# Performance work log

Hardware: AMD Instinct MI355X
Metric: run time of the kernel (lower is better)

The kernel has to match this reference:

```python
import jax, jax.numpy as jnp
import numpy as np

EMBED = 1024
HEAD = 64
SEQ = 2048
BATCH = 8


def setup_inputs() -> dict:
    key = jax.random.key(0)
    kx, kq, kk, kv = jax.random.split(key, 4)
    x = jax.random.normal(kx, (BATCH, SEQ, EMBED), dtype=jnp.float32)
    # torch nn.Linear weight is [out,in]; we store [in,out] so y = x @ W
    Wq = jax.random.normal(kq, (EMBED, HEAD), dtype=jnp.float32) * (EMBED ** -0.5)
    Wk = jax.random.normal(kk, (EMBED, HEAD), dtype=jnp.float32) * (EMBED ** -0.5)
    Wv = jax.random.normal(kv, (EMBED, HEAD), dtype=jnp.float32) * (EMBED ** -0.5)
    return {"x": x, "Wq": Wq, "Wk": Wk, "Wv": Wv}


def reference(x, Wq, Wk, Wv):
    # x: [B,T,C]; single-head causal attention. Scale uses C (embedding dim),
    # matching the original module's C ** (-0.5). Dropout in eval mode (identity).
    B, T, C = x.shape
    q = x @ Wq  # [B,T,H]
    k = x @ Wk  # [B,T,H]
    v = x @ Wv  # [B,T,H]
    scores = jnp.einsum('bqh,bkh->bqk', q, k) * (C ** -0.5)  # [B,T,T]
    causal = jnp.tril(jnp.ones((T, T), dtype=bool))
    scores = jnp.where(causal, scores, -jnp.inf)
    weights = jax.nn.softmax(scores, axis=-1)
    return jnp.einsum('bqk,bkh->bqh', weights, v)  # [B,T,H]
```

## Files before the change

### kernel.cpp

```cpp
#include <hip/hip_runtime.h>
#include <hip/hip_bf16.h>
#include <math.h>

#define BATCH 8
#define SEQ 2048
#define EMBED 1024
#define HEAD 64
#define NROWS (BATCH*SEQ)

typedef short bf16x8 __attribute__((ext_vector_type(8)));
typedef short bf16x4 __attribute__((ext_vector_type(4)));
typedef float f32x4  __attribute__((ext_vector_type(4)));

__device__ inline short f2bf(float f) {
    __hip_bfloat16 h = __float2bfloat16(f);
    return *(short*)&h;
}
__device__ inline float bf2f(short s) {
    __hip_bfloat16 h = *(__hip_bfloat16*)&s;
    return __bfloat162float(h);
}

#define NSLOT 144
__device__ __host__ inline int triOff(int qt) {
    int g = qt >> 2;
    return 2 * g * (g + 1) + (qt & 3) * (g + 1);
}

__global__ __launch_bounds__(256) void prep_w(
    const float* __restrict__ Wq, const float* __restrict__ Wk,
    const float* __restrict__ Wv, short* __restrict__ wt)
{
    int g    = blockIdx.x * 256 + threadIdx.x;
    int lane = g & 63;
    int frag = g >> 6;
    int k32  = frag & 31;
    int ct   = frag >> 5;
    int col  = ct * 16 + (lane & 15);
    int mm   = col >> 6, cc = col & 63;
    const float* W = (mm == 0) ? Wq : ((mm == 1) ? Wk : Wv);
    int kb = k32 * 32 + (lane >> 4) * 8;
    bf16x8 o;
#pragma unroll
    for (int j = 0; j < 8; j++)
        o[j] = f2bf(W[(size_t)(kb + j) * HEAD + cc]);
    *(bf16x8*)&wt[(size_t)g * 8] = o;
}

__global__ __launch_bounds__(512, 4) void proj_kernel(
    const float* __restrict__ x, const short* __restrict__ wt,
    short* __restrict__ q, short* __restrict__ k, short* __restrict__ v)
{
    __shared__ short xs[32][1024];
    float* psum = (float*)&xs[0][0];

    const int tid  = threadIdx.x;
    const int wave = tid >> 6, lane = tid & 63;
    const int m16  = lane & 15, quad = lane >> 4;
    const int cg   = wave & 3;
    const int kh   = wave >> 2;
    const int r0   = blockIdx.x * 32;

    {
        const int row  = tid >> 4;
        const int col4 = tid & 15;
        const float* xr = x + (size_t)(r0 + row) * EMBED;
#pragma unroll
        for (int h = 0; h < 2; h++) {
            float4 f[8];
#pragma unroll
            for (int i = 0; i < 8; i++)
                f[i] = *(const float4*)&xr[(h * 8 + i) * 64 + col4 * 4];
#pragma unroll
            for (int i = 0; i < 8; i++) {
                int c  = (h * 8 + i) * 64 + col4 * 4;
                int k8 = c >> 3, rem = c & 7;
                int cs = ((k8 ^ (row & 7)) << 3) + rem;
                bf16x4 bv;
                bv[0] = f2bf(f[i].x); bv[1] = f2bf(f[i].y);
                bv[2] = f2bf(f[i].z); bv[3] = f2bf(f[i].w);
                *(bf16x4*)&xs[row][cs] = bv;
            }
        }
    }
    __syncthreads();

    f32x4 acc[2][3];
#pragma unroll
    for (int mt = 0; mt < 2; mt++)
#pragma unroll
        for (int j = 0; j < 3; j++) acc[mt][j] = (f32x4){0.f, 0.f, 0.f, 0.f};

#pragma unroll 4
    for (int s = 0; s < 16; s++) {
        int k32  = kh * 16 + s;
        int ksw  = ((k32 * 4 + quad) ^ (m16 & 7)) << 3;
        bf16x8 a0 = *(const bf16x8*)&xs[m16][ksw];
        bf16x8 a1 = *(const bf16x8*)&xs[16 + m16][ksw];
#pragma unroll
        for (int j = 0; j < 3; j++) {
            int ct = cg * 3 + j;
            bf16x8 bb = *(const bf16x8*)&wt[(size_t)((ct * 32 + k32) * 64 + lane) * 8];
            acc[0][j] = __builtin_amdgcn_mfma_f32_16x16x32_bf16(a0, bb, acc[0][j], 0, 0, 0);
            acc[1][j] = __builtin_amdgcn_mfma_f32_16x16x32_bf16(a1, bb, acc[1][j], 0, 0, 0);
        }
    }

    __syncthreads();
    if (kh == 1) {
        float* p = psum + ((size_t)(cg * 64 + lane) * 24);
#pragma unroll
        for (int mt = 0; mt < 2; mt++)
#pragma unroll
            for (int j = 0; j < 3; j++)
                *(f32x4*)&p[(mt * 3 + j) * 4] = acc[mt][j];
    }
    __syncthreads();
    if (kh == 0) {
        const float* p = psum + ((size_t)(cg * 64 + lane) * 24);
#pragma unroll
        for (int mt = 0; mt < 2; mt++)
#pragma unroll
            for (int j = 0; j < 3; j++) {
                f32x4 o = acc[mt][j] + *(const f32x4*)&p[(mt * 3 + j) * 4];
                int gcol = (cg * 3 + j) * 16 + m16;
                int mm = gcol >> 6, cc = gcol & 63;
                short* op = (mm == 0) ? q : ((mm == 1) ? k : v);
#pragma unroll
                for (int reg = 0; reg < 4; reg++) {
                    int row = r0 + mt * 16 + quad * 4 + reg;
                    op[(size_t)row * HEAD + cc] = f2bf(o[reg]);
                }
            }
    }
}

__global__ __launch_bounds__(256) void attn_kernel(
    const short* __restrict__ qg, const short* __restrict__ kg,
    const short* __restrict__ vg,
    short* __restrict__ pO, float* __restrict__ pl)
{
    __shared__ short ksh[64][88];
    __shared__ short vsh[64][88];
    __shared__ short psh[4][16][88];

    const int qt  = blockIdx.x;
    const int seg = blockIdx.y;
    const int b   = blockIdx.z;
    const int c0  = seg * 4;
    const int c1  = min(seg * 4 + 4, qt + 1);
    if (c0 >= c1) return;

    const int tid  = threadIdx.x;
    const int wave = tid >> 6, lane = tid & 63;
    const int m16  = lane & 15, quad = lane >> 4;
    const float scale = 0.03125f;

    const short* qb = qg + (size_t)b * SEQ * HEAD;
    const short* kb = kg + (size_t)b * SEQ * HEAD;
    const short* vb = vg + (size_t)b * SEQ * HEAD;

    bf16x8 a_q[2];
    {
        const int qrow = qt * 64 + wave * 16 + m16;
        a_q[0] = *(const bf16x8*)&qb[(size_t)qrow * HEAD + quad * 8];
        a_q[1] = *(const bf16x8*)&qb[(size_t)qrow * HEAD + 32 + quad * 8];
    }

    f32x4 o_acc[4];
#pragma unroll
    for (int i = 0; i < 4; i++) o_acc[i] = (f32x4){0.f, 0.f, 0.f, 0.f};
    float lsum[4] = {0.f, 0.f, 0.f, 0.f};

    const int krow = tid >> 3;
    const int ks8  = tid & 7;
    const int vp0  = tid >> 3;
    const int vh0  = (tid & 7) * 8;
    const int vpp  = vp0 ^ ((tid & 7) << 2);

    bf16x8 kr0 = *(const bf16x8*)&kb[(size_t)(c0 * 64 + krow) * HEAD + ks8 * 8];
    bf16x8 kr1 = *(const bf16x8*)&kb[(size_t)(c0 * 64 + 32 + krow) * HEAD + ks8 * 8];
    bf16x8 vr0 = *(const bf16x8*)&vb[(size_t)(c0 * 64 + 2 * vp0) * HEAD + vh0];
    bf16x8 vr1 = *(const bf16x8*)&vb[(size_t)(c0 * 64 + 2 * vp0 + 1) * HEAD + vh0];

    for (int c = c0; c < c1; c++) {
        const int t0 = c * 64;
        __syncthreads();
        {
            *(bf16x8*)&ksh[krow][ks8 * 8]      = kr0;
            *(bf16x8*)&ksh[32 + krow][ks8 * 8] = kr1;
#pragma unroll
            for (int j = 0; j < 8; j++) {
                int hh = vh0 + j;
                int val = (vr0[j] & 0xffff) | (((int)vr1[j]) << 16);
                *(int*)&vsh[hh][vpp * 2] = val;
            }
        }
        __syncthreads();
        if (c + 1 < c1) {
            const int tn = (c + 1) * 64;
            kr0 = *(const bf16x8*)&kb[(size_t)(tn + krow) * HEAD + ks8 * 8];
            kr1 = *(const bf16x8*)&kb[(size_t)(tn + 32 + krow) * HEAD + ks8 * 8];
            vr0 = *(const bf16x8*)&vb[(size_t)(tn + 2 * vp0) * HEAD + vh0];
            vr1 = *(const bf16x8*)&vb[(size_t)(tn + 2 * vp0 + 1) * HEAD + vh0];
        }

        f32x4 s_t[4];
#pragma unroll
        for (int nt = 0; nt < 4; nt++) {
            bf16x8 bk0 = *(const bf16x8*)&ksh[nt * 16 + m16][quad * 8];
            bf16x8 bk1 = *(const bf16x8*)&ksh[nt * 16 + m16][32 + quad * 8];
            f32x4 acc = (f32x4){0.f, 0.f, 0.f, 0.f};
            acc = __builtin_amdgcn_mfma_f32_16x16x32_bf16(a_q[0], bk0, acc, 0, 0, 0);
            acc = __builtin_amdgcn_mfma_f32_16x16x32_bf16(a_q[1], bk1, acc, 0, 0, 0);
            s_t[nt] = acc;
        }

        if (c == qt) {
#pragma unroll
            for (int r = 0; r < 4; r++) {
                const int row = qt * 64 + wave * 16 + quad * 4 + r;
#pragma unroll
                for (int nt = 0; nt < 4; nt++) {
                    int t = t0 + nt * 16 + m16;
                    float p = (t <= row) ? __expf(s_t[nt][r] * scale) : 0.f;
                    lsum[r] += p;
                    psh[wave][quad * 4 + r][nt * 16 + m16] = f2bf(p);
                }
            }
        } else {
#pragma unroll
            for (int r = 0; r < 4; r++) {
#pragma unroll
                for (int nt = 0; nt < 4; nt++) {
                    float p = __expf(s_t[nt][r] * scale);
                    lsum[r] += p;
                    psh[wave][quad * 4 + r][nt * 16 + m16] = f2bf(p);
                }
            }
        }

#pragma unroll
        for (int s = 0; s < 2; s++) {
            bf16x8 a_p = *(const bf16x8*)&psh[wave][m16][s * 32 + quad * 8];
#pragma unroll
            for (int ht = 0; ht < 4; ht++) {
                int hh = ht * 16 + m16;
                int pb = (s * 16 + quad * 4) ^ (((hh >> 3) & 7) << 2);
                bf16x8 b_v = *(const bf16x8*)&vsh[hh][pb * 2];
                o_acc[ht] = __builtin_amdgcn_mfma_f32_16x16x32_bf16(a_p, b_v, o_acc[ht], 0, 0, 0);
            }
        }
    }

#pragma unroll
    for (int r = 0; r < 4; r++) {
#pragma unroll
        for (int off = 8; off >= 1; off >>= 1)
            lsum[r] += __shfl_xor(lsum[r], off, 64);
    }
    const size_t slot  = (size_t)b * NSLOT + triOff(qt) + seg;
    const size_t pbase = slot * 64;
#pragma unroll
    for (int ht = 0; ht < 4; ht++) {
#pragma unroll
        for (int r = 0; r < 4; r++) {
            int rowt = wave * 16 + quad * 4 + r;
            pO[(pbase + rowt) * 64 + ht * 16 + m16] = f2bf(o_acc[ht][r]);
        }
    }
    if (m16 == 0) {
#pragma unroll
        for (int r = 0; r < 4; r++) {
            int rowt = wave * 16 + quad * 4 + r;
            pl[pbase + rowt] = lsum[r];
        }
    }
}

__global__ __launch_bounds__(256) void combine_kernel(
    const short* __restrict__ pO, const float* __restrict__ pl,
    float* __restrict__ out)
{
    int g   = blockIdx.x * 256 + threadIdx.x;
    int h4  = (g & 15) * 4;
    int row = (g >> 4) & 2047;
    int b   = g >> 15;
    int qt  = row >> 6, lr = row & 63;
    int ns  = (qt >> 2) + 1;
    size_t base = (size_t)b * NSLOT + triOff(qt);
    float4 O = {0.f, 0.f, 0.f, 0.f};
    float  L = 0.f;
    for (int s = 0; s < ns; s++) {
        bf16x4 ov = *(const bf16x4*)&pO[((base + s) * 64 + lr) * 64 + h4];
        O.x += bf2f(ov[0]); O.y += bf2f(ov[1]);
        O.z += bf2f(ov[2]); O.w += bf2f(ov[3]);
        L += pl[(base + s) * 64 + lr];
    }
    float inv = 1.f / L;
    O.x *= inv; O.y *= inv; O.z *= inv; O.w *= inv;
    *(float4*)&out[(size_t)g * 4] = O;
}

extern "C" void kernel_launch(void* const* d_in, const int* in_sizes, int n_in,
                              void* d_out, int out_size, void* d_ws, size_t ws_size,
                              hipStream_t stream) {
    const float* x  = (const float*)d_in[0];
    const float* Wq = (const float*)d_in[1];
    const float* Wk = (const float*)d_in[2];
    const float* Wv = (const float*)d_in[3];
    float* out = (float*)d_out;

    short* q  = (short*)d_ws;
    short* k  = q + (size_t)NROWS * HEAD;
    short* v  = k + (size_t)NROWS * HEAD;
    short* wt = v + (size_t)NROWS * HEAD;
    short* pO = wt + 196608;
    float* pl = (float*)(pO + (size_t)BATCH * NSLOT * 64 * 64);

    prep_w<<<96, 256, 0, stream>>>(Wq, Wk, Wv, wt);
    proj_kernel<<<512, 512, 0, stream>>>(x, wt, q, k, v);
    attn_kernel<<<dim3(32, 8, 8), 256, 0, stream>>>(q, k, v, pO, pl);
    combine_kernel<<<1024, 256, 0, stream>>>(pO, pl, out);
}
```

Baseline: 128.9 us.

## Store V transposed and read K/V directly from global, dropping LDS staging

The projection kernel now writes V in a transposed [B,H,T] layout, so the attention kernel can load V fragments for the PV MFMA directly from global memory with contiguous vector loads. The LDS staging of K and V, along with the per-tile __syncthreads barriers, is removed and each wave reads K/V itself through the cache. Partial outputs are re-indexed per 16-row wave tile. This removes block barriers and LDS traffic, but every wave in a block now fetches the same K/V tiles redundantly from L1/L2, and the transposed V store in proj is a 4-element strided write.

```diff
diff --git a/kernel.cpp b/kernel.cpp
--- a/kernel.cpp
+++ b/kernel.cpp
@@ -21,10 +21,10 @@
     return __bfloat162float(h);
 }
 
-#define NSLOT 144
-__device__ __host__ inline int triOff(int qt) {
-    int g = qt >> 2;
-    return 2 * g * (g + 1) + (qt & 3) * (g + 1);
+#define NSLOT16 576
+__device__ inline int triOff16(int qtile) {
+    int g = qtile >> 4;
+    return qtile + 8 * g * (g - 1) + (qtile & 15) * g;
 }
 
 __global__ __launch_bounds__(256) void prep_w(
@@ -49,7 +49,7 @@
 
 __global__ __launch_bounds__(512, 4) void proj_kernel(
     const float* __restrict__ x, const short* __restrict__ wt,
-    short* __restrict__ q, short* __restrict__ k, short* __restrict__ v)
+    short* __restrict__ q, short* __restrict__ k, short* __restrict__ vt)
 {
     __shared__ short xs[32][1024];
     float* psum = (float*)&xs[0][0];
@@ -118,6 +118,8 @@
     __syncthreads();
     if (kh == 0) {
         const float* p = psum + ((size_t)(cg * 64 + lane) * 24);
+        const int bb = r0 >> 11;
+        const int tb = r0 & 2047;
 #pragma unroll
         for (int mt = 0; mt < 2; mt++)
 #pragma unroll
@@ -125,11 +127,19 @@
                 f32x4 o = acc[mt][j] + *(const f32x4*)&p[(mt * 3 + j) * 4];
                 int gcol = (cg * 3 + j) * 16 + m16;
                 int mm = gcol >> 6, cc = gcol & 63;
-                short* op = (mm == 0) ? q : ((mm == 1) ? k : v);
-#pragma unroll
-                for (int reg = 0; reg < 4; reg++) {
-                    int row = r0 + mt * 16 + quad * 4 + reg;
-                    op[(size_t)row * HEAD + cc] = f2bf(o[reg]);
+                if (mm < 2) {
+                    short* op = (mm == 0) ? q : k;
+#pragma unroll
+                    for (int reg = 0; reg < 4; reg++) {
+                        int row = r0 + mt * 16 + quad * 4 + reg;
+                        op[(size_t)row * HEAD + cc] = f2bf(o[reg]);
+                    }
+                } else {
+                    bf16x4 pk;
+                    pk[0] = f2bf(o[0]); pk[1] = f2bf(o[1]);
+                    pk[2] = f2bf(o[2]); pk[3] = f2bf(o[3]);
+                    int t = tb + mt * 16 + quad * 4;
+                    *(bf16x4*)&vt[(((size_t)bb * 64 + cc) << 11) + t] = pk;
                 }
             }
     }
@@ -137,34 +147,32 @@
 
 __global__ __launch_bounds__(256) void attn_kernel(
     const short* __restrict__ qg, const short* __restrict__ kg,
-    const short* __restrict__ vg,
+    const short* __restrict__ vtg,
     short* __restrict__ pO, float* __restrict__ pl)
 {
-    __shared__ short ksh[64][88];
-    __shared__ short vsh[64][88];
-    __shared__ short psh[4][16][88];
-
-    const int qt  = blockIdx.x;
-    const int seg = blockIdx.y;
-    const int b   = blockIdx.z;
-    const int c0  = seg * 4;
-    const int c1  = min(seg * 4 + 4, qt + 1);
+    __shared__ short psh[4][16][72];
+
+    const int qt64 = blockIdx.x;
+    const int seg  = blockIdx.y;
+    const int b    = blockIdx.z;
+    const int c0 = seg * 4;
+    const int c1 = min(seg * 4 + 4, qt64 + 1);
     if (c0 >= c1) return;
 
-    const int tid  = threadIdx.x;
-    const int wave = tid >> 6, lane = tid & 63;
+    const int wave = threadIdx.x >> 6, lane = threadIdx.x & 63;
     const int m16  = lane & 15, quad = lane >> 4;
+    const int qtile = qt64 * 4 + wave;
     const float scale = 0.03125f;
 
-    const short* qb = qg + (size_t)b * SEQ * HEAD;
-    const short* kb = kg + (size_t)b * SEQ * HEAD;
-    const short* vb = vg + (size_t)b * SEQ * HEAD;
-
-    bf16x8 a_q[2];
+    const short* qb  = qg  + (size_t)b * SEQ * HEAD;
+    const short* kb  = kg  + (size_t)b * SEQ * HEAD;
+    const short* vtb = vtg + (size_t)b * HEAD * SEQ;
+
+    bf16x8 a_q0, a_q1;
     {
-        const int qrow = qt * 64 + wave * 16 + m16;
-        a_q[0] = *(const bf16x8*)&qb[(size_t)qrow * HEAD + quad * 8];
-        a_q[1] = *(const bf16x8*)&qb[(size_t)qrow * HEAD + 32 + quad * 8];
+        const int qrow = qtile * 16 + m16;
+        a_q0 = *(const bf16x8*)&qb[(size_t)qrow * HEAD + quad * 8];
+        a_q1 = *(const bf16x8*)&qb[(size_t)qrow * HEAD + 32 + quad * 8];
     }
 
     f32x4 o_acc[4];
@@ -172,54 +180,25 @@
     for (int i = 0; i < 4; i++) o_acc[i] = (f32x4){0.f, 0.f, 0.f, 0.f};
     float lsum[4] = {0.f, 0.f, 0.f, 0.f};
 
-    const int krow = tid >> 3;
-    const int ks8  = tid & 7;
-    const int vp0  = tid >> 3;
-    const int vh0  = (tid & 7) * 8;
-    const int vpp  = vp0 ^ ((tid & 7) << 2);
-
-    bf16x8 kr0 = *(const bf16x8*)&kb[(size_t)(c0 * 64 + krow) * HEAD + ks8 * 8];
-    bf16x8 kr1 = *(const bf16x8*)&kb[(size_t)(c0 * 64 + 32 + krow) * HEAD + ks8 * 8];
-    bf16x8 vr0 = *(const bf16x8*)&vb[(size_t)(c0 * 64 + 2 * vp0) * HEAD + vh0];
-    bf16x8 vr1 = *(const bf16x8*)&vb[(size_t)(c0 * 64 + 2 * vp0 + 1) * HEAD + vh0];
-
     for (int c = c0; c < c1; c++) {
         const int t0 = c * 64;
-        __syncthreads();
-        {
-            *(bf16x8*)&ksh[krow][ks8 * 8]      = kr0;
-            *(bf16x8*)&ksh[32 + krow][ks8 * 8] = kr1;
-#pragma unroll
-            for (int j = 0; j < 8; j++) {
-                int hh = vh0 + j;
-                int val = (vr0[j] & 0xffff) | (((int)vr1[j]) << 16);
-                *(int*)&vsh[hh][vpp * 2] = val;
-            }
-        }
-        __syncthreads();
-        if (c + 1 < c1) {
-            const int tn = (c + 1) * 64;
-            kr0 = *(const bf16x8*)&kb[(size_t)(tn + krow) * HEAD + ks8 * 8];
-            kr1 = *(const bf16x8*)&kb[(size_t)(tn + 32 + krow) * HEAD + ks8 * 8];
-            vr0 = *(const bf16x8*)&vb[(size_t)(tn + 2 * vp0) * HEAD + vh0];
-            vr1 = *(const bf16x8*)&vb[(size_t)(tn + 2 * vp0 + 1) * HEAD + vh0];
-        }
 
         f32x4 s_t[4];
 #pragma unroll
         for (int nt = 0; nt < 4; nt++) {
-            bf16x8 bk0 = *(const bf16x8*)&ksh[nt * 16 + m16][quad * 8];
-            bf16x8 bk1 = *(const bf16x8*)&ksh[nt * 16 + m16][32 + quad * 8];
+            const short* kr = &kb[(size_t)(t0 + nt * 16 + m16) * HEAD + quad * 8];
+            bf16x8 bk0 = *(const bf16x8*)kr;
+            bf16x8 bk1 = *(const bf16x8*)(kr + 32);
             f32x4 acc = (f32x4){0.f, 0.f, 0.f, 0.f};
-            acc = __builtin_amdgcn_mfma_f32_16x16x32_bf16(a_q[0], bk0, acc, 0, 0, 0);
-            acc = __builtin_amdgcn_mfma_f32_16x16x32_bf16(a_q[1], bk1, acc, 0, 0, 0);
+            acc = __builtin_amdgcn_mfma_f32_16x16x32_bf16(a_q0, bk0, acc, 0, 0, 0);
+            acc = __builtin_amdgcn_mfma_f32_16x16x32_bf16(a_q1, bk1, acc, 0, 0, 0);
             s_t[nt] = acc;
         }
 
-        if (c == qt) {
+        if (c == qt64) {
 #pragma unroll
             for (int r = 0; r < 4; r++) {
-                const int row = qt * 64 + wave * 16 + quad * 4 + r;
+                const int row = qtile * 16 + quad * 4 + r;
 #pragma unroll
                 for (int nt = 0; nt < 4; nt++) {
                     int t = t0 + nt * 16 + m16;
@@ -246,8 +225,7 @@
 #pragma unroll
             for (int ht = 0; ht < 4; ht++) {
                 int hh = ht * 16 + m16;
-                int pb = (s * 16 + quad * 4) ^ (((hh >> 3) & 7) << 2);
-                bf16x8 b_v = *(const bf16x8*)&vsh[hh][pb * 2];
+                bf16x8 b_v = *(const bf16x8*)&vtb[((size_t)hh << 11) + t0 + s * 32 + quad * 8];
                 o_acc[ht] = __builtin_amdgcn_mfma_f32_16x16x32_bf16(a_p, b_v, o_acc[ht], 0, 0, 0);
             }
         }
@@ -259,20 +237,20 @@
         for (int off = 8; off >= 1; off >>= 1)
             lsum[r] += __shfl_xor(lsum[r], off, 64);
     }
-    const size_t slot  = (size_t)b * NSLOT + triOff(qt) + seg;
-    const size_t pbase = slot * 64;
+    const size_t slot = (size_t)b * NSLOT16 + triOff16(qtile) + (seg - 0);
+    const size_t pbase = slot * 16;
 #pragma unroll
     for (int ht = 0; ht < 4; ht++) {
 #pragma unroll
         for (int r = 0; r < 4; r++) {
-            int rowt = wave * 16 + quad * 4 + r;
+            int rowt = quad * 4 + r;
             pO[(pbase + rowt) * 64 + ht * 16 + m16] = f2bf(o_acc[ht][r]);
         }
     }
     if (m16 == 0) {
 #pragma unroll
         for (int r = 0; r < 4; r++) {
-            int rowt = wave * 16 + quad * 4 + r;
+            int rowt = quad * 4 + r;
             pl[pbase + rowt] = lsum[r];
         }
     }
@@ -282,20 +260,20 @@
     const short* __restrict__ pO, const float* __restrict__ pl,
     float* __restrict__ out)
 {
-    int g   = blockIdx.x * 256 + threadIdx.x;
-    int h4  = (g & 15) * 4;
-    int row = (g >> 4) & 2047;
-    int b   = g >> 15;
-    int qt  = row >> 6, lr = row & 63;
-    int ns  = (qt >> 2) + 1;
-    size_t base = (size_t)b * NSLOT + triOff(qt);
+    int g    = blockIdx.x * 256 + threadIdx.x;
+    int h4   = (g & 15) * 4;
+    int row  = (g >> 4) & 2047;
+    int b    = g >> 15;
+    int qtile = row >> 4, rowt = row & 15;
+    int ns   = (qtile >> 4) + 1;
+    size_t base = (size_t)b * NSLOT16 + triOff16(qtile);
     float4 O = {0.f, 0.f, 0.f, 0.f};
     float  L = 0.f;
     for (int s = 0; s < ns; s++) {
-        bf16x4 ov = *(const bf16x4*)&pO[((base + s) * 64 + lr) * 64 + h4];
+        bf16x4 ov = *(const bf16x4*)&pO[((base + s) * 16 + rowt) * 64 + h4];
         O.x += bf2f(ov[0]); O.y += bf2f(ov[1]);
         O.z += bf2f(ov[2]); O.w += bf2f(ov[3]);
-        L += pl[(base + s) * 64 + lr];
+        L += pl[(base + s) * 16 + rowt];
     }
     float inv = 1.f / L;
     O.x *= inv; O.y *= inv; O.z *= inv; O.w *= inv;
@@ -313,13 +291,13 @@
 
     short* q  = (short*)d_ws;
     short* k  = q + (size_t)NROWS * HEAD;
-    short* v  = k + (size_t)NROWS * HEAD;
-    short* wt = v + (size_t)NROWS * HEAD;
+    short* vt = k + (size_t)NROWS * HEAD;
+    short* wt = vt + (size_t)NROWS * HEAD;
     short* pO = wt + 196608;
-    float* pl = (float*)(pO + (size_t)BATCH * NSLOT * 64 * 64);
+    float* pl = (float*)(pO + (size_t)BATCH * NSLOT16 * 16 * 64);
 
     prep_w<<<96, 256, 0, stream>>>(Wq, Wk, Wv, wt);
-    proj_kernel<<<512, 512, 0, stream>>>(x, wt, q, k, v);
-    attn_kernel<<<dim3(32, 8, 8), 256, 0, stream>>>(q, k, v, pO, pl);
+    proj_kernel<<<512, 512, 0, stream>>>(x, wt, q, k, vt);
+    attn_kernel<<<dim3(32, 8, 8), 256, 0, stream>>>(q, k, vt, pO, pl);
     combine_kernel<<<1024, 256, 0, stream>>>(pO, pl, out);
 }
```

Result: slower. 176.1 us (+36.6%).
